# Kernel tuning notes

Hardware: AMD Instinct MI355X
Metric: run time of the kernel (lower is better)

Reference implementation:

```python
import jax, jax.numpy as jnp
import numpy as np

DIM = 96
HEADS = 6
WS = 8                      # window_size
OWS = int(WS * 0.5) + WS    # overlap_win_size = 12
PAD = (OWS - WS) // 2       # 2
Dd = Hh = Ww = 24
B = 1
L = Dd * Hh * Ww
MLP_H = DIM * 2
TBL = (WS + OWS - 1) ** 3   # 6859 relative-position-bias entries


def setup_inputs() -> dict:
    key = jax.random.key(0)
    ks = jax.random.split(key, 8)
    def n(k, shape, s=0.02):
        return jax.random.normal(k, shape, jnp.float32) * s
    return {
        "x": jax.random.normal(ks[0], (B, L, DIM), jnp.float32),
        "ln1_w": jnp.ones((DIM,), jnp.float32),
        "ln1_b": jnp.zeros((DIM,), jnp.float32),
        "qkv_w": n(ks[1], (3 * DIM, DIM)),
        "qkv_b": jnp.zeros((3 * DIM,), jnp.float32),
        "rpb": n(ks[2], (TBL, HEADS)),
        "proj_w": n(ks[3], (DIM, DIM)),
        "proj_b": jnp.zeros((DIM,), jnp.float32),
        "ln2_w": jnp.ones((DIM,), jnp.float32),
        "ln2_b": jnp.zeros((DIM,), jnp.float32),
        "fc1_w": n(ks[4], (MLP_H, DIM)),
        "fc1_b": jnp.zeros((MLP_H,), jnp.float32),
        "fc2_w": n(ks[5], (DIM, MLP_H)),
        "fc2_b": jnp.zeros((DIM,), jnp.float32),
        "rpi": jax.random.randint(ks[6], (WS ** 3, OWS ** 3), 0, TBL),
        "D": Dd, "H": Hh, "W": Ww,
    }


def _ln(x, w, b):
    m = jnp.mean(x, -1, keepdims=True)
    v = jnp.var(x, -1, keepdims=True)
    return (x - m) / jnp.sqrt(v + 1e-5) * w + b


def _ocab3d(x, ln1_w, ln1_b, qkv_w, qkv_b, rpb, proj_w, proj_b,
            ln2_w, ln2_b, fc1_w, fc1_b, fc2_w, fc2_b, rpi, D, H, W):
    Bz, Lz, C = x.shape
    hd = C // HEADS
    scale = hd ** -0.5
    shortcut = x

    xn = _ln(x, ln1_w, ln1_b).reshape(Bz, D, H, W, C)
    qkv = xn @ qkv_w.T + qkv_b                   # [B,D,H,W,3C]
    q = qkv[..., :C]
    kv = qkv[..., C:]                            # cat(k, v) on channels, [B,D,H,W,2C]

    nD, nH, nW = D // WS, H // WS, W // WS
    nw = nD * nH * nW

    # non-overlapping query windows -> [B*nw, WS^3, C]
    qw = q.reshape(Bz, nD, WS, nH, WS, nW, WS, C)
    qw = qw.transpose(0, 1, 3, 5, 2, 4, 6, 7).reshape(Bz * nw, WS ** 3, C)

    # overlapping kv windows via pad + strided gather (mirrors F.pad + unfold)
    kvp = jnp.pad(kv, ((0, 0), (PAD, PAD), (PAD, PAD), (PAD, PAD), (0, 0)))
    idx_d = (jnp.arange(nD) * WS)[:, None] + jnp.arange(OWS)[None, :]
    idx_h = (jnp.arange(nH) * WS)[:, None] + jnp.arange(OWS)[None, :]
    idx_w = (jnp.arange(nW) * WS)[:, None] + jnp.arange(OWS)[None, :]
    kw = kvp[:, idx_d]                 # [B,nD,OWS,Hp,Wp,2C]
    kw = kw[:, :, :, idx_h]            # [B,nD,OWS,nH,OWS,Wp,2C]
    kw = kw[:, :, :, :, :, idx_w]      # [B,nD,OWS,nH,OWS,nW,OWS,2C]
    kw = kw.transpose(0, 1, 3, 5, 2, 4, 6, 7).reshape(Bz * nw, OWS ** 3, 2 * C)
    kk, vv = kw[..., :C], kw[..., C:]

    qh = qw.reshape(-1, WS ** 3, HEADS, hd).transpose(0, 2, 1, 3) * scale
    kh = kk.reshape(-1, OWS ** 3, HEADS, hd).transpose(0, 2, 1, 3)
    vh = vv.reshape(-1, OWS ** 3, HEADS, hd).transpose(0, 2, 1, 3)

    attn = jnp.einsum('bhqd,bhkd->bhqk', qh, kh)               # [B*nw,H,512,1728]
    bias = rpb[rpi.reshape(-1)].reshape(WS ** 3, OWS ** 3, HEADS).transpose(2, 0, 1)
    attn = jax.nn.softmax(attn + bias[None], axis=-1)
    out = jnp.einsum('bhqk,bhkd->bhqd', attn, vh)
    out = out.transpose(0, 2, 1, 3).reshape(Bz * nw, WS ** 3, C)

    # window reverse -> [B, L, C]
    out = out.reshape(Bz, nD, nH, nW, WS, WS, WS, C)
    out = out.transpose(0, 1, 4, 2, 5, 3, 6, 7).reshape(Bz, D * H * W, C)

    x2 = out @ proj_w.T + proj_b + shortcut
    h1 = jax.nn.gelu(_ln(x2, ln2_w, ln2_b) @ fc1_w.T + fc1_b, approximate=False)
    return x2 + (h1 @ fc2_w.T + fc2_b)


def reference(x, ln1_w, ln1_b, qkv_w, qkv_b, rpb, proj_w, proj_b,
              ln2_w, ln2_b, fc1_w, fc1_b, fc2_w, fc2_b, rpi, D, H, W):
    return _ocab3d(x, ln1_w, ln1_b, qkv_w, qkv_b, rpb, proj_w, proj_b,
                   ln2_w, ln2_b, fc1_w, fc1_b, fc2_w, fc2_b, rpi, D, H, W)
```

## Files before the change

kernel.cpp:

```cpp
#include <hip/hip_runtime.h>
#include <math.h>

#define DIMC   96
#define NHEADS 6
#define HD     16
#define WSZ    8
#define OWSZ   12
#define PADW   2
#define DD     24
#define LTOK   13824
#define NWIN   27
#define NKEY   1728
#define NROW   512
#define MLPH   192
#define PDIM   28
#define PD3    21952
#define KVPN   (NHEADS*PD3*32)
#define TBL    6859
#define LSTR   82944
#define AOSTR  1327104

typedef __attribute__((ext_vector_type(4))) short bf16x4;
typedef __attribute__((ext_vector_type(8))) short bf16x8;
typedef __attribute__((ext_vector_type(4))) float f32x4;

__device__ __forceinline__ unsigned short bfround(float f) {
    unsigned u = __float_as_uint(f);
    return (unsigned short)((u + 0x7FFFu + ((u >> 16) & 1u)) >> 16);
}
__device__ __forceinline__ unsigned bfpack(float a, float b) {
    unsigned ua = __float_as_uint(a), ub = __float_as_uint(b);
    ua = (ua + 0x7FFFu + ((ua >> 16) & 1u)) >> 16;
    ub = (ub + 0x7FFFu + ((ub >> 16) & 1u)) >> 16;
    return ua | (ub << 16);
}
__device__ __forceinline__ uint4 pack8(const float* v) {
    uint4 u;
    u.x = bfpack(v[0], v[1]); u.y = bfpack(v[2], v[3]);
    u.z = bfpack(v[4], v[5]); u.w = bfpack(v[6], v[7]);
    return u;
}
__device__ __forceinline__ bf16x4 pack4(f32x4 p) {
    union { uint2 u; bf16x4 v; } r;
    r.u.x = __builtin_amdgcn_perm(__float_as_uint(p[1]), __float_as_uint(p[0]), 0x07060302u);
    r.u.y = __builtin_amdgcn_perm(__float_as_uint(p[3]), __float_as_uint(p[2]), 0x07060302u);
    return r.v;
}
__device__ __forceinline__ f32x4 mfma16(bf16x4 a, bf16x4 b, f32x4 c) {
#if __has_builtin(__builtin_amdgcn_mfma_f32_16x16x16bf16_1k)
    return __builtin_amdgcn_mfma_f32_16x16x16bf16_1k(a, b, c, 0, 0, 0);
#else
    bf16x8 a8 = {a[0], a[1], a[2], a[3], 0, 0, 0, 0};
    bf16x8 b8 = {b[0], b[1], b[2], b[3], 0, 0, 0, 0};
    return __builtin_amdgcn_mfma_f32_16x16x32_bf16(a8, b8, c, 0, 0, 0);
#endif
}

#define ZBLK 2058
__global__ __launch_bounds__(256) void init_kernel(
        float4* __restrict__ kvz, const float* __restrict__ rpb,
        float* __restrict__ rpbT) {
    int bx = blockIdx.x;
    if (bx < ZBLK) {
        int i = bx * 256 + threadIdx.x;
        if (i < KVPN * 2 / 16) kvz[i] = make_float4(0.f, 0.f, 0.f, 0.f);
    } else {
        int i = (bx - ZBLK) * 256 + threadIdx.x;
        if (i < TBL) {
            #pragma unroll
            for (int h = 0; h < NHEADS; ++h) rpbT[h * TBL + i] = rpb[i * NHEADS + h];
        }
    }
}

template<int KT, int MODE, bool LN, int NSPLIT>
__global__ __launch_bounds__(256) void gemm_kernel(
        const float* __restrict__ X, const float* __restrict__ W,
        const float* __restrict__ bias, const float* __restrict__ lnw,
        const float* __restrict__ lnb, const float* __restrict__ res,
        const float* __restrict__ X2, const float* __restrict__ lbuf,
        void* __restrict__ out, void* __restrict__ out2) {
    constexpr int K = KT * 32;
    __shared__ uint4 Af4[2 * KT * 4 * 16];
    __shared__ uint4 Bf4[6 * KT * 4 * 16];
    int tid  = threadIdx.x;
    int nc   = blockIdx.x % NSPLIT;
    int row0 = (blockIdx.x / NSPLIT) * 32;

    if (tid < 128) {
        int row = tid >> 2, part = tid & 3;
        int rt = row >> 4, mm = row & 15;
        if (MODE == 1) {
            int grow = row0 + row;
            const float4* a0 = (const float4*)(X  + (long)grow * 96 + part * 24);
            const float4* a1 = (const float4*)(X2 + (long)grow * 96 + part * 24);
            int ha = (part * 3) >> 1, hb = ha + 1;
            float inva = 1.f / (lbuf[grow*6 + ha] + lbuf[LSTR + grow*6 + ha]);
            float invb = 1.f / (lbuf[grow*6 + hb] + lbuf[LSTR + grow*6 + hb]);
            float v[24];
            #pragma unroll
            for (int i = 0; i < 6; ++i) {
                float4 u0 = a0[i], u1 = a1[i];
                #pragma unroll
                for (int j = 0; j < 4; ++j) {
                    int gc = part * 24 + i * 4 + j;
                    float lv = ((gc >> 4) == ha) ? inva : invb;
                    float s = (j==0?u0.x+u1.x : j==1?u0.y+u1.y : j==2?u0.z+u1.z : u0.w+u1.w);
                    v[i*4+j] = s * lv;
                }
            }
            #pragma unroll
            for (int gg = 0; gg < 3; ++gg) {
                int g = part * 3 + gg;
                int kt = g >> 2, qq = g & 3;
                Af4[((rt * KT + kt) * 4 + qq) * 16 + mm] = pack8(v + gg * 8);
            }
        } else if (LN) {
            float v[24];
            const float4* xp = (const float4*)(X + (long)(row0 + row) * K + part * 24);
            float s = 0.f, sq = 0.f;
            #pragma unroll
            for (int i = 0; i < 6; ++i) {
                float4 t = xp[i];
                v[i*4+0] = t.x; v[i*4+1] = t.y; v[i*4+2] = t.z; v[i*4+3] = t.w;
                s  += t.x + t.y + t.z + t.w;
                sq += t.x*t.x + t.y*t.y + t.z*t.z + t.w*t.w;
            }
            s  += __shfl_xor(s, 1);  s  += __shfl_xor(s, 2);
            sq += __shfl_xor(sq, 1); sq += __shfl_xor(sq, 2);
            float mean = s * (1.f / 96.f);
            float inv  = rsqrtf(sq * (1.f / 96.f) - mean * mean + 1e-5f);
            const float4* wp = (const float4*)(lnw + part * 24);
            const float4* bp = (const float4*)(lnb + part * 24);
            #pragma unroll
            for (int i = 0; i < 6; ++i) {
                float4 wv = wp[i], bv = bp[i];
                v[i*4+0] = (v[i*4+0] - mean) * inv * wv.x + bv.x;
                v[i*4+1] = (v[i*4+1] - mean) * inv * wv.y + bv.y;
                v[i*4+2] = (v[i*4+2] - mean) * inv * wv.z + bv.z;
                v[i*4+3] = (v[i*4+3] - mean) * inv * wv.w + bv.w;
            }
            #pragma unroll
            for (int gg = 0; gg < 3; ++gg) {
                int g = part * 3 + gg;
                int kt = g >> 2, qq = g & 3;
                Af4[((rt * KT + kt) * 4 + qq) * 16 + mm] = pack8(v + gg * 8);
            }
        } else {
            const float* xr = X + (long)(row0 + row) * K + part * (K / 4);
            #pragma unroll
            for (int gg = 0; gg < KT; ++gg) {
                const float4* xp = (const float4*)(xr + gg * 8);
                float v[8];
                float4 t0 = xp[0], t1 = xp[1];
                v[0]=t0.x; v[1]=t0.y; v[2]=t0.z; v[3]=t0.w;
                v[4]=t1.x; v[5]=t1.y; v[6]=t1.z; v[7]=t1.w;
                int g = part * KT + gg;
                int kt = g >> 2, qq = g & 3;
                Af4[((rt * KT + kt) * 4 + qq) * 16 + mm] = pack8(v);
            }
        }
    }

    for (int idx = tid; idx < 96 * 4 * KT; idx += 256) {
        int n = idx / (4 * KT);
        int g = idx % (4 * KT);
        const float4* wp = (const float4*)(W + (long)(nc * 96 + n) * K + g * 8);
        float v[8];
        float4 t0 = wp[0], t1 = wp[1];
        v[0]=t0.x; v[1]=t0.y; v[2]=t0.z; v[3]=t0.w;
        v[4]=t1.x; v[5]=t1.y; v[6]=t1.z; v[7]=t1.w;
        int ct = n >> 4, nn = n & 15, kt = g >> 2, qg = g & 3;
        Bf4[((ct * KT + kt) * 4 + qg) * 16 + nn] = pack8(v);
    }
    __syncthreads();

    int wave = tid >> 6, lane = tid & 63;
    int qq = lane >> 4, mI = lane & 15;
    int rt = wave & 1, cg = wave >> 1;

    f32x4 acc[3];
    #pragma unroll
    for (int j = 0; j < 3; ++j) acc[j] = (f32x4){0.f, 0.f, 0.f, 0.f};
    #pragma unroll
    for (int kt = 0; kt < KT; ++kt) {
        bf16x8 a = *(const bf16x8*)&Af4[((rt * KT + kt) * 4 + qq) * 16 + mI];
        #pragma unroll
        for (int j = 0; j < 3; ++j) {
            bf16x8 b = *(const bf16x8*)&Bf4[(((cg * 3 + j) * KT + kt) * 4 + qq) * 16 + mI];
            acc[j] = __builtin_amdgcn_mfma_f32_16x16x32_bf16(a, b, acc[j], 0, 0, 0);
        }
    }

    float bv[3];
    #pragma unroll
    for (int j = 0; j < 3; ++j) bv[j] = bias[nc * 96 + (cg * 3 + j) * 16 + mI];
    #pragma unroll
    for (int r = 0; r < 4; ++r) {
        int row = row0 + rt * 16 + qq * 4 + r;
        if (MODE == 0) {
            if (nc == 0) {
                unsigned short* op = (unsigned short*)out + (long)row * 96;
                #pragma unroll
                for (int j = 0; j < 3; ++j)
                    op[(cg * 3 + j) * 16 + mI] = bfround(0.25f * (acc[j][r] + bv[j]));
            } else {
                int d = row / 576, hh = (row / 24) % 24, w2 = row % 24;
                long pos = ((long)(d + 2) * 28 + (hh + 2)) * 28 + (w2 + 2);
                #pragma unroll
                for (int j = 0; j < 3; ++j) {
                    int head = cg * 3 + j;
                    ((unsigned short*)out2)[((long)head * PD3 + pos) * 32 +
                        (nc == 2 ? 16 : 0) + mI] = bfround(acc[j][r] + bv[j]);
                }
            }
        } else if (MODE == 1 || MODE == 3) {
            const float* rp = res + (long)row * 96;
            float* op = (float*)out + (long)row * 96;
            #pragma unroll
            for (int j = 0; j < 3; ++j)
                op[(cg * 3 + j) * 16 + mI] = acc[j][r] + bv[j] + rp[(cg * 3 + j) * 16 + mI];
        } else {
            float* op = (float*)out + (long)row * 192 + nc * 96;
            #pragma unroll
            for (int j = 0; j < 3; ++j) {
                float v = acc[j][r] + bv[j];
                op[(cg * 3 + j) * 16 + mI] = 0.5f * v * (1.f + erff(v * 0.70710678f));
            }
        }
    }
}

__global__ __launch_bounds__(256) void bias_kernel(
        const int* __restrict__ rpi, const float* __restrict__ rpbT,
        float* __restrict__ biasP) {
    int bx = blockIdx.x;
    int head = bx / 216;
    int r2 = bx % 216;
    int kt = r2 >> 1, qh = r2 & 1;
    const float* tab = rpbT + head * TBL;
    int k0 = kt * 16;
    int qi = qh * 256 + threadIdx.x;
    const int* rp = rpi + (long)qi * NKEY + k0;
    int idx[16];
    #pragma unroll
    for (int j = 0; j < 4; ++j) {
        int4 t = *(const int4*)(rp + j * 4);
        idx[j*4+0] = t.x; idx[j*4+1] = t.y; idx[j*4+2] = t.z; idx[j*4+3] = t.w;
    }
    #pragma unroll
    for (int quad = 0; quad < 4; ++quad) {
        float4 v;
        v.x = tab[idx[quad*4+0]];
        v.y = tab[idx[quad*4+1]];
        v.z = tab[idx[quad*4+2]];
        v.w = tab[idx[quad*4+3]];
        *(float4*)(biasP + ((((long)head*108 + kt)*4 + quad)*512 + qi)*4) = v;
    }
}

#define KSTR 20
#define VSTR 68
__global__ __launch_bounds__(256) void attn_kernel(
        const unsigned short* __restrict__ q, const unsigned short* __restrict__ kvp2,
        const float* __restrict__ biasP, float* __restrict__ ao,
        float* __restrict__ lbuf) {
    __shared__ unsigned short Ks[2][64 * KSTR];
    __shared__ unsigned short Vs[2][16 * VSTR];
    int bid = blockIdx.x;
    int w = bid / 48, rem = bid % 48;
    int head = rem >> 3;
    int quart = (rem >> 1) & 3, half = rem & 1;
    int wd8 = (w / 9) * 8, wh8 = ((w / 3) % 3) * 8, ww8 = (w % 3) * 8;
    int tid = threadIdx.x, wave = tid >> 6, lane = tid & 63;
    int quad = lane >> 4, m16 = lane & 15;
    int key = tid >> 2, part = tid & 3;
    int c0 = half ? 13 : 0;
    int cn = half ? 14 : 13;

    auto kvaddr = [&](int c) -> const uint4* {
        int jg = c * 64 + key;
        int i = jg / 144, jh = (jg / 12) % 12, jw = jg % 12;
        long sp = ((long)(wd8 + i) * PDIM + (wh8 + jh)) * PDIM + (ww8 + jw);
        return (const uint4*)(kvp2 + ((long)head * PD3 + sp) * 32 + part * 8);
    };
    auto writeLDS = [&](int b, uint4 v) {
        if (part < 2) {
            *(uint2*)(&Ks[b][key * KSTR + part * 8])     = make_uint2(v.x, v.y);
            *(uint2*)(&Ks[b][key * KSTR + part * 8 + 4]) = make_uint2(v.z, v.w);
        } else {
            int d0 = (part - 2) * 8;
            Vs[b][(d0+0)*VSTR + key] = (unsigned short)(v.x);
            Vs[b][(d0+1)*VSTR + key] = (unsigned short)(v.x >> 16);
            Vs[b][(d0+2)*VSTR + key] = (unsigned short)(v.y);
            Vs[b][(d0+3)*VSTR + key] = (unsigned short)(v.y >> 16);
            Vs[b][(d0+4)*VSTR + key] = (unsigned short)(v.z);
            Vs[b][(d0+5)*VSTR + key] = (unsigned short)(v.z >> 16);
            Vs[b][(d0+6)*VSTR + key] = (unsigned short)(v.w);
            Vs[b][(d0+7)*VSTR + key] = (unsigned short)(v.w >> 16);
        }
    };

    int grow[2]; bf16x4 qf[2];
    #pragma unroll
    for (int qt = 0; qt < 2; ++qt) {
        int ql = quart * 128 + wave * 32 + qt * 16 + m16;
        int ld = ql >> 6, lh = (ql >> 3) & 7, lw = ql & 7;
        grow[qt] = ((wd8 + ld) * 24 + (wh8 + lh)) * 24 + (ww8 + lw);
        qf[qt] = *(const bf16x4*)(q + (long)grow[qt] * 96 + head * 16 + quad * 4);
    }

    const float* bbase = biasP + (long)head * 884736 + quad * 2048
                         + ((quart * 128 + wave * 32 + m16) << 2);
    f32x4 bcur[2][4];
    #pragma unroll
    for (int qt = 0; qt < 2; ++qt)
        #pragma unroll
        for (int kt = 0; kt < 4; ++kt)
            bcur[qt][kt] = *(const f32x4*)(bbase + (long)(c0*4 + kt) * 8192 + qt * 64);

    writeLDS(0, *kvaddr(c0));

    f32x4 o[2];
    o[0] = (f32x4){0.f,0.f,0.f,0.f}; o[1] = (f32x4){0.f,0.f,0.f,0.f};
    float l[2] = {0.f, 0.f};
    uint4 stgn;

    #pragma unroll 1
    for (int cc = 0; cc < cn; ++cc) {
        int c = c0 + cc;
        if (cc + 1 < cn) stgn = *kvaddr(c + 1);
        __syncthreads();
        int b = cc & 1;

        bf16x4 kf[4];
        #pragma unroll
        for (int kt = 0; kt < 4; ++kt)
            kf[kt] = *(const bf16x4*)(&Ks[b][(kt * 16 + m16) * KSTR + quad * 4]);

        f32x4 S[2][4];
        #pragma unroll
        for (int qt = 0; qt < 2; ++qt)
            #pragma unroll
            for (int kt = 0; kt < 4; ++kt)
                S[qt][kt] = mfma16(kf[kt], qf[qt], bcur[qt][kt]);

        f32x4 bnxt[2][4];
        if (cc + 1 < cn) {
            const float* bp = bbase + (long)(c + 1) * 32768;
            #pragma unroll
            for (int qt = 0; qt < 2; ++qt)
                #pragma unroll
                for (int kt = 0; kt < 4; ++kt)
                    bnxt[qt][kt] = *(const f32x4*)(bp + kt * 8192 + qt * 64);
        }

        #pragma unroll
        for (int qt = 0; qt < 2; ++qt) {
            float ls = 0.f;
            #pragma unroll
            for (int kt = 0; kt < 4; ++kt)
                #pragma unroll
                for (int r = 0; r < 4; ++r) {
                    float p = __expf(S[qt][kt][r]);
                    S[qt][kt][r] = p; ls += p;
                }
            l[qt] += ls;
        }

        #pragma unroll
        for (int kt = 0; kt < 4; ++kt) {
            bf16x4 vf = *(const bf16x4*)(&Vs[b][m16 * VSTR + kt * 16 + quad * 4]);
            o[0] = mfma16(vf, pack4(S[0][kt]), o[0]);
            o[1] = mfma16(vf, pack4(S[1][kt]), o[1]);
        }

        if (cc + 1 < cn) writeLDS((cc + 1) & 1, stgn);
        #pragma unroll
        for (int qt = 0; qt < 2; ++qt)
            #pragma unroll
            for (int kt = 0; kt < 4; ++kt) bcur[qt][kt] = bnxt[qt][kt];
    }

    float* aout = ao + (long)half * AOSTR;
    float* lout = lbuf + (long)half * LSTR;
    #pragma unroll
    for (int qt = 0; qt < 2; ++qt) {
        float lq = l[qt];
        lq += __shfl_xor(lq, 16);
        lq += __shfl_xor(lq, 32);
        float4* op = (float4*)(aout + (long)grow[qt] * 96 + head * 16 + quad * 4);
        *op = make_float4(o[qt][0], o[qt][1], o[qt][2], o[qt][3]);
        if (quad == 0) lout[grow[qt] * 6 + head] = lq;
    }
}

extern "C" void kernel_launch(void* const* d_in, const int* in_sizes, int n_in,
                              void* d_out, int out_size, void* d_ws, size_t ws_size,
                              hipStream_t stream) {
    const float* x     = (const float*)d_in[0];
    const float* ln1w  = (const float*)d_in[1];
    const float* ln1b  = (const float*)d_in[2];
    const float* qkvw  = (const float*)d_in[3];
    const float* qkvb  = (const float*)d_in[4];
    const float* rpb   = (const float*)d_in[5];
    const float* projw = (const float*)d_in[6];
    const float* projb = (const float*)d_in[7];
    const float* ln2w  = (const float*)d_in[8];
    const float* ln2b  = (const float*)d_in[9];
    const float* fc1w  = (const float*)d_in[10];
    const float* fc1b  = (const float*)d_in[11];
    const float* fc2w  = (const float*)d_in[12];
    const float* fc2b  = (const float*)d_in[13];
    const int*   rpi   = (const int*)d_in[14];
    float* outp = (float*)d_out;

    float* ws = (float*)d_ws;
    float*          aop    = ws;
    unsigned short* q16    = (unsigned short*)(ws + 2654208);
    unsigned short* kvp16  = (unsigned short*)(ws + 3317760);
    float*          biasPf = ws + 5425152;
    float*          hbuf   = biasPf;
    float*          rpbT   = ws + 10733568;
    float*          lbuf   = ws + 10774722;
    float*          x2     = aop;

    init_kernel<<<ZBLK + 27, 256, 0, stream>>>((float4*)kvp16, rpb, rpbT);
    gemm_kernel<3, 0, true , 3><<<1296, 256, 0, stream>>>(x,  qkvw, qkvb, ln1w, ln1b, nullptr, nullptr, nullptr, q16, kvp16);
    bias_kernel<<<1296, 256, 0, stream>>>(rpi, rpbT, biasPf);
    attn_kernel<<<NWIN * NHEADS * 4 * 2, 256, 0, stream>>>(q16, kvp16, biasPf, aop, lbuf);
    gemm_kernel<3, 1, false, 1><<<432, 256, 0, stream>>>(aop, projw, projb, nullptr, nullptr, x, aop + AOSTR, lbuf, x2, nullptr);
    gemm_kernel<3, 2, true , 2><<<864, 256, 0, stream>>>(x2, fc1w, fc1b, ln2w, ln2b, nullptr, nullptr, nullptr, hbuf, nullptr);
    gemm_kernel<6, 3, false, 1><<<432, 256, 0, stream>>>(hbuf, fc2w, fc2b, nullptr, nullptr, x2, nullptr, nullptr, outp, nullptr);
}
```

Before: 190.9 us.

## Fuse proj/LN2/MLP into one kernel, store bias in bf16, remap attention blocks

Merges the three post-attention GEMM launches (proj+residual, LN2+fc1+GELU, fc2+residual) into one mlp_kernel that keeps x2 and the GELU activations in shared memory, so the x2 and hidden buffers no longer round-trip through global memory. The precomputed relative-position bias is now stored as bf16 instead of fp32, halving the bytes the attention kernel streams. The attention grid is also remapped so consecutive blocks on the same XCD share windows and heads, which may improve L2 reuse. The trade-offs are lower bias precision and a fused kernel with more syncs and more LDS use per block.

Measured after the change: 186.7 us. -2.2%, faster.

```diff
diff --git a/kernel.cpp b/kernel.cpp
--- a/kernel.cpp
+++ b/kernel.cpp
@@ -73,99 +73,56 @@
     }
 }
 
-template<int KT, int MODE, bool LN, int NSPLIT>
-__global__ __launch_bounds__(256) void gemm_kernel(
+template<int KT>
+__global__ __launch_bounds__(256) void qkv_kernel(
         const float* __restrict__ X, const float* __restrict__ W,
         const float* __restrict__ bias, const float* __restrict__ lnw,
-        const float* __restrict__ lnb, const float* __restrict__ res,
-        const float* __restrict__ X2, const float* __restrict__ lbuf,
-        void* __restrict__ out, void* __restrict__ out2) {
-    constexpr int K = KT * 32;
+        const float* __restrict__ lnb,
+        unsigned short* __restrict__ out, unsigned short* __restrict__ out2) {
     __shared__ uint4 Af4[2 * KT * 4 * 16];
     __shared__ uint4 Bf4[6 * KT * 4 * 16];
     int tid  = threadIdx.x;
-    int nc   = blockIdx.x % NSPLIT;
-    int row0 = (blockIdx.x / NSPLIT) * 32;
+    int nc   = blockIdx.x % 3;
+    int row0 = (blockIdx.x / 3) * 32;
 
     if (tid < 128) {
         int row = tid >> 2, part = tid & 3;
         int rt = row >> 4, mm = row & 15;
-        if (MODE == 1) {
-            int grow = row0 + row;
-            const float4* a0 = (const float4*)(X  + (long)grow * 96 + part * 24);
-            const float4* a1 = (const float4*)(X2 + (long)grow * 96 + part * 24);
-            int ha = (part * 3) >> 1, hb = ha + 1;
-            float inva = 1.f / (lbuf[grow*6 + ha] + lbuf[LSTR + grow*6 + ha]);
-            float invb = 1.f / (lbuf[grow*6 + hb] + lbuf[LSTR + grow*6 + hb]);
-            float v[24];
-            #pragma unroll
-            for (int i = 0; i < 6; ++i) {
-                float4 u0 = a0[i], u1 = a1[i];
-                #pragma unroll
-                for (int j = 0; j < 4; ++j) {
-                    int gc = part * 24 + i * 4 + j;
-                    float lv = ((gc >> 4) == ha) ? inva : invb;
-                    float s = (j==0?u0.x+u1.x : j==1?u0.y+u1.y : j==2?u0.z+u1.z : u0.w+u1.w);
-                    v[i*4+j] = s * lv;
-                }
-            }
-            #pragma unroll
-            for (int gg = 0; gg < 3; ++gg) {
-                int g = part * 3 + gg;
-                int kt = g >> 2, qq = g & 3;
-                Af4[((rt * KT + kt) * 4 + qq) * 16 + mm] = pack8(v + gg * 8);
-            }
-        } else if (LN) {
-            float v[24];
-            const float4* xp = (const float4*)(X + (long)(row0 + row) * K + part * 24);
-            float s = 0.f, sq = 0.f;
-            #pragma unroll
-            for (int i = 0; i < 6; ++i) {
-                float4 t = xp[i];
-                v[i*4+0] = t.x; v[i*4+1] = t.y; v[i*4+2] = t.z; v[i*4+3] = t.w;
-                s  += t.x + t.y + t.z + t.w;
-                sq += t.x*t.x + t.y*t.y + t.z*t.z + t.w*t.w;
-            }
-            s  += __shfl_xor(s, 1);  s  += __shfl_xor(s, 2);
-            sq += __shfl_xor(sq, 1); sq += __shfl_xor(sq, 2);
-            float mean = s * (1.f / 96.f);
-            float inv  = rsqrtf(sq * (1.f / 96.f) - mean * mean + 1e-5f);
-            const float4* wp = (const float4*)(lnw + part * 24);
-            const float4* bp = (const float4*)(lnb + part * 24);
-            #pragma unroll
-            for (int i = 0; i < 6; ++i) {
-                float4 wv = wp[i], bv = bp[i];
-                v[i*4+0] = (v[i*4+0] - mean) * inv * wv.x + bv.x;
-                v[i*4+1] = (v[i*4+1] - mean) * inv * wv.y + bv.y;
-                v[i*4+2] = (v[i*4+2] - mean) * inv * wv.z + bv.z;
-                v[i*4+3] = (v[i*4+3] - mean) * inv * wv.w + bv.w;
-            }
-            #pragma unroll
-            for (int gg = 0; gg < 3; ++gg) {
-                int g = part * 3 + gg;
-                int kt = g >> 2, qq = g & 3;
-                Af4[((rt * KT + kt) * 4 + qq) * 16 + mm] = pack8(v + gg * 8);
-            }
-        } else {
-            const float* xr = X + (long)(row0 + row) * K + part * (K / 4);
-            #pragma unroll
-            for (int gg = 0; gg < KT; ++gg) {
-                const float4* xp = (const float4*)(xr + gg * 8);
-                float v[8];
-                float4 t0 = xp[0], t1 = xp[1];
-                v[0]=t0.x; v[1]=t0.y; v[2]=t0.z; v[3]=t0.w;
-                v[4]=t1.x; v[5]=t1.y; v[6]=t1.z; v[7]=t1.w;
-                int g = part * KT + gg;
-                int kt = g >> 2, qq = g & 3;
-                Af4[((rt * KT + kt) * 4 + qq) * 16 + mm] = pack8(v);
-            }
-        }
-    }
-
+        float v[24];
+        const float4* xp = (const float4*)(X + (long)(row0 + row) * 96 + part * 24);
+        float s = 0.f, sq = 0.f;
+        #pragma unroll
+        for (int i = 0; i < 6; ++i) {
+            float4 t = xp[i];
+            v[i*4+0] = t.x; v[i*4+1] = t.y; v[i*4+2] = t.z; v[i*4+3] = t.w;
+            s  += t.x + t.y + t.z + t.w;
+            sq += t.x*t.x + t.y*t.y + t.z*t.z + t.w*t.w;
+        }
+        s  += __shfl_xor(s, 1);  s  += __shfl_xor(s, 2);
+        sq += __shfl_xor(sq, 1); sq += __shfl_xor(sq, 2);
+        float mean = s * (1.f / 96.f);
+        float inv  = rsqrtf(sq * (1.f / 96.f) - mean * mean + 1e-5f);
+        const float4* wp = (const float4*)(lnw + part * 24);
+        const float4* bp = (const float4*)(lnb + part * 24);
+        #pragma unroll
+        for (int i = 0; i < 6; ++i) {
+            float4 wv = wp[i], bv = bp[i];
+            v[i*4+0] = (v[i*4+0] - mean) * inv * wv.x + bv.x;
+            v[i*4+1] = (v[i*4+1] - mean) * inv * wv.y + bv.y;
+            v[i*4+2] = (v[i*4+2] - mean) * inv * wv.z + bv.z;
+            v[i*4+3] = (v[i*4+3] - mean) * inv * wv.w + bv.w;
+        }
+        #pragma unroll
+        for (int gg = 0; gg < 3; ++gg) {
+            int g = part * 3 + gg;
+            int kt = g >> 2, qq = g & 3;
+            Af4[((rt * KT + kt) * 4 + qq) * 16 + mm] = pack8(v + gg * 8);
+        }
+    }
     for (int idx = tid; idx < 96 * 4 * KT; idx += 256) {
         int n = idx / (4 * KT);
         int g = idx % (4 * KT);
-        const float4* wp = (const float4*)(W + (long)(nc * 96 + n) * K + g * 8);
+        const float4* wp = (const float4*)(W + (long)(nc * 96 + n) * 96 + g * 8);
         float v[8];
         float4 t0 = wp[0], t1 = wp[1];
         v[0]=t0.x; v[1]=t0.y; v[2]=t0.z; v[3]=t0.w;
@@ -198,34 +155,19 @@
     #pragma unroll
     for (int r = 0; r < 4; ++r) {
         int row = row0 + rt * 16 + qq * 4 + r;
-        if (MODE == 0) {
-            if (nc == 0) {
-                unsigned short* op = (unsigned short*)out + (long)row * 96;
-                #pragma unroll
-                for (int j = 0; j < 3; ++j)
-                    op[(cg * 3 + j) * 16 + mI] = bfround(0.25f * (acc[j][r] + bv[j]));
-            } else {
-                int d = row / 576, hh = (row / 24) % 24, w2 = row % 24;
-                long pos = ((long)(d + 2) * 28 + (hh + 2)) * 28 + (w2 + 2);
-                #pragma unroll
-                for (int j = 0; j < 3; ++j) {
-                    int head = cg * 3 + j;
-                    ((unsigned short*)out2)[((long)head * PD3 + pos) * 32 +
-                        (nc == 2 ? 16 : 0) + mI] = bfround(acc[j][r] + bv[j]);
-                }
-            }
-        } else if (MODE == 1 || MODE == 3) {
-            const float* rp = res + (long)row * 96;
-            float* op = (float*)out + (long)row * 96;
+        if (nc == 0) {
+            unsigned short* op = out + (long)row * 96;
             #pragma unroll
             for (int j = 0; j < 3; ++j)
-                op[(cg * 3 + j) * 16 + mI] = acc[j][r] + bv[j] + rp[(cg * 3 + j) * 16 + mI];
+                op[(cg * 3 + j) * 16 + mI] = bfround(0.25f * (acc[j][r] + bv[j]));
         } else {
-            float* op = (float*)out + (long)row * 192 + nc * 96;
+            int d = row / 576, hh = (row / 24) % 24, w2 = row % 24;
+            long pos = ((long)(d + 2) * 28 + (hh + 2)) * 28 + (w2 + 2);
             #pragma unroll
             for (int j = 0; j < 3; ++j) {
-                float v = acc[j][r] + bv[j];
-                op[(cg * 3 + j) * 16 + mI] = 0.5f * v * (1.f + erff(v * 0.70710678f));
+                int head = cg * 3 + j;
+                out2[((long)head * PD3 + pos) * 32 +
+                     (nc == 2 ? 16 : 0) + mI] = bfround(acc[j][r] + bv[j]);
             }
         }
     }
@@ -233,7 +175,7 @@
 
 __global__ __launch_bounds__(256) void bias_kernel(
         const int* __restrict__ rpi, const float* __restrict__ rpbT,
-        float* __restrict__ biasP) {
+        unsigned short* __restrict__ biasP) {
     int bx = blockIdx.x;
     int head = bx / 216;
     int r2 = bx % 216;
@@ -250,12 +192,12 @@
     }
     #pragma unroll
     for (int quad = 0; quad < 4; ++quad) {
-        float4 v;
-        v.x = tab[idx[quad*4+0]];
-        v.y = tab[idx[quad*4+1]];
-        v.z = tab[idx[quad*4+2]];
-        v.w = tab[idx[quad*4+3]];
-        *(float4*)(biasP + ((((long)head*108 + kt)*4 + quad)*512 + qi)*4) = v;
+        ushort4 v;
+        v.x = bfround(tab[idx[quad*4+0]]);
+        v.y = bfround(tab[idx[quad*4+1]]);
+        v.z = bfround(tab[idx[quad*4+2]]);
+        v.w = bfround(tab[idx[quad*4+3]]);
+        *(ushort4*)(biasP + ((((long)head*108 + kt)*4 + quad)*512 + qi)*4) = v;
     }
 }
 
@@ -263,14 +205,19 @@
 #define VSTR 68
 __global__ __launch_bounds__(256) void attn_kernel(
         const unsigned short* __restrict__ q, const unsigned short* __restrict__ kvp2,
-        const float* __restrict__ biasP, float* __restrict__ ao,
+        const unsigned short* __restrict__ biasP, float* __restrict__ ao,
         float* __restrict__ lbuf) {
     __shared__ unsigned short Ks[2][64 * KSTR];
     __shared__ unsigned short Vs[2][16 * VSTR];
     int bid = blockIdx.x;
-    int w = bid / 48, rem = bid % 48;
-    int head = rem >> 3;
-    int quart = (rem >> 1) & 3, half = rem & 1;
+    int xcd = bid & 7, slot = bid >> 3;
+    int L = xcd * 162 + slot;
+    int head = L / 216;
+    int rem = L % 216;
+    int half = rem / 108;
+    int r3 = rem % 108;
+    int quart = r3 / 27;
+    int w = r3 % 27;
     int wd8 = (w / 9) * 8, wh8 = ((w / 3) % 3) * 8, ww8 = (w % 3) * 8;
     int tid = threadIdx.x, wave = tid >> 6, lane = tid & 63;
     int quad = lane >> 4, m16 = lane & 15;
@@ -310,14 +257,14 @@
         qf[qt] = *(const bf16x4*)(q + (long)grow[qt] * 96 + head * 16 + quad * 4);
     }
 
-    const float* bbase = biasP + (long)head * 884736 + quad * 2048
-                         + ((quart * 128 + wave * 32 + m16) << 2);
-    f32x4 bcur[2][4];
+    const unsigned short* bbase = biasP + (long)head * 884736 + quad * 2048
+                                  + ((quart * 128 + wave * 32 + m16) << 2);
+    uint2 bcur[2][4];
     #pragma unroll
     for (int qt = 0; qt < 2; ++qt)
         #pragma unroll
         for (int kt = 0; kt < 4; ++kt)
-            bcur[qt][kt] = *(const f32x4*)(bbase + (long)(c0*4 + kt) * 8192 + qt * 64);
+            bcur[qt][kt] = *(const uint2*)(bbase + (long)(c0*4 + kt) * 8192 + qt * 64);
 
     writeLDS(0, *kvaddr(c0));
 
@@ -342,17 +289,24 @@
         #pragma unroll
         for (int qt = 0; qt < 2; ++qt)
             #pragma unroll
-            for (int kt = 0; kt < 4; ++kt)
-                S[qt][kt] = mfma16(kf[kt], qf[qt], bcur[qt][kt]);
-
-        f32x4 bnxt[2][4];
+            for (int kt = 0; kt < 4; ++kt) {
+                uint2 bv = bcur[qt][kt];
+                f32x4 ci;
+                ci[0] = __uint_as_float(bv.x << 16);
+                ci[1] = __uint_as_float(bv.x & 0xffff0000u);
+                ci[2] = __uint_as_float(bv.y << 16);
+                ci[3] = __uint_as_float(bv.y & 0xffff0000u);
+                S[qt][kt] = mfma16(kf[kt], qf[qt], ci);
+            }
+
+        uint2 bnxt[2][4];
         if (cc + 1 < cn) {
-            const float* bp = bbase + (long)(c + 1) * 32768;
+            const unsigned short* bp = bbase + (long)(c + 1) * 32768;
             #pragma unroll
             for (int qt = 0; qt < 2; ++qt)
                 #pragma unroll
                 for (int kt = 0; kt < 4; ++kt)
-                    bnxt[qt][kt] = *(const f32x4*)(bp + kt * 8192 + qt * 64);
+                    bnxt[qt][kt] = *(const uint2*)(bp + kt * 8192 + qt * 64);
         }
 
         #pragma unroll
@@ -392,6 +346,216 @@
         float4* op = (float4*)(aout + (long)grow[qt] * 96 + head * 16 + quad * 4);
         *op = make_float4(o[qt][0], o[qt][1], o[qt][2], o[qt][3]);
         if (quad == 0) lout[grow[qt] * 6 + head] = lq;
+    }
+}
+
+__global__ __launch_bounds__(256) void mlp_kernel(
+        const float* __restrict__ ao0, const float* __restrict__ ao1,
+        const float* __restrict__ lbuf,
+        const float* __restrict__ projw, const float* __restrict__ projb,
+        const float* __restrict__ x,
+        const float* __restrict__ ln2w, const float* __restrict__ ln2b,
+        const float* __restrict__ fc1w, const float* __restrict__ fc1b,
+        const float* __restrict__ fc2w, const float* __restrict__ fc2b,
+        float* __restrict__ out) {
+    __shared__ uint4 Af4[2 * 3 * 4 * 16];
+    __shared__ uint4 Bf4[6 * 3 * 4 * 16];
+    __shared__ float x2s[32 * 96];
+    __shared__ unsigned short h16[32 * 192];
+    int tid = threadIdx.x;
+    int row0 = blockIdx.x * 32;
+    int wave = tid >> 6, lane = tid & 63;
+    int qq = lane >> 4, mI = lane & 15;
+    int rt = wave & 1, cg = wave >> 1;
+
+    if (tid < 128) {
+        int row = tid >> 2, part = tid & 3;
+        int rtA = row >> 4, mm = row & 15;
+        int grow = row0 + row;
+        const float4* a0 = (const float4*)(ao0 + (long)grow * 96 + part * 24);
+        const float4* a1 = (const float4*)(ao1 + (long)grow * 96 + part * 24);
+        int ha = (part * 3) >> 1, hb = ha + 1;
+        float inva = 1.f / (lbuf[grow*6 + ha] + lbuf[LSTR + grow*6 + ha]);
+        float invb = 1.f / (lbuf[grow*6 + hb] + lbuf[LSTR + grow*6 + hb]);
+        float v[24];
+        #pragma unroll
+        for (int i = 0; i < 6; ++i) {
+            float4 u0 = a0[i], u1 = a1[i];
+            #pragma unroll
+            for (int j = 0; j < 4; ++j) {
+                int gc = part * 24 + i * 4 + j;
+                float lv = ((gc >> 4) == ha) ? inva : invb;
+                float s = (j==0?u0.x+u1.x : j==1?u0.y+u1.y : j==2?u0.z+u1.z : u0.w+u1.w);
+                v[i*4+j] = s * lv;
+            }
+        }
+        #pragma unroll
+        for (int gg = 0; gg < 3; ++gg) {
+            int g = part * 3 + gg;
+            int kt = g >> 2, q4 = g & 3;
+            Af4[((rtA * 3 + kt) * 4 + q4) * 16 + mm] = pack8(v + gg * 8);
+        }
+    }
+    for (int idx = tid; idx < 96 * 12; idx += 256) {
+        int n = idx / 12, g = idx % 12;
+        const float4* wp = (const float4*)(projw + (long)n * 96 + g * 8);
+        float v[8];
+        float4 t0 = wp[0], t1 = wp[1];
+        v[0]=t0.x; v[1]=t0.y; v[2]=t0.z; v[3]=t0.w;
+        v[4]=t1.x; v[5]=t1.y; v[6]=t1.z; v[7]=t1.w;
+        int ct = n >> 4, nn = n & 15, kt = g >> 2, qg = g & 3;
+        Bf4[((ct * 3 + kt) * 4 + qg) * 16 + nn] = pack8(v);
+    }
+    __syncthreads();
+
+    {
+        f32x4 acc[3];
+        #pragma unroll
+        for (int j = 0; j < 3; ++j) acc[j] = (f32x4){0.f,0.f,0.f,0.f};
+        #pragma unroll
+        for (int kt = 0; kt < 3; ++kt) {
+            bf16x8 a = *(const bf16x8*)&Af4[((rt * 3 + kt) * 4 + qq) * 16 + mI];
+            #pragma unroll
+            for (int j = 0; j < 3; ++j) {
+                bf16x8 b = *(const bf16x8*)&Bf4[(((cg * 3 + j) * 3 + kt) * 4 + qq) * 16 + mI];
+                acc[j] = __builtin_amdgcn_mfma_f32_16x16x32_bf16(a, b, acc[j], 0, 0, 0);
+            }
+        }
+        float bv[3];
+        #pragma unroll
+        for (int j = 0; j < 3; ++j) bv[j] = projb[(cg * 3 + j) * 16 + mI];
+        #pragma unroll
+        for (int r = 0; r < 4; ++r) {
+            int row = rt * 16 + qq * 4 + r;
+            int grow = row0 + row;
+            #pragma unroll
+            for (int j = 0; j < 3; ++j) {
+                int col = (cg * 3 + j) * 16 + mI;
+                x2s[row * 96 + col] = acc[j][r] + bv[j] + x[(long)grow * 96 + col];
+            }
+        }
+    }
+    __syncthreads();
+
+    if (tid < 128) {
+        int row = tid >> 2, part = tid & 3;
+        int rtA = row >> 4, mm = row & 15;
+        float v[24];
+        const float4* xp = (const float4*)(x2s + row * 96 + part * 24);
+        float s = 0.f, sq = 0.f;
+        #pragma unroll
+        for (int i = 0; i < 6; ++i) {
+            float4 t = xp[i];
+            v[i*4+0] = t.x; v[i*4+1] = t.y; v[i*4+2] = t.z; v[i*4+3] = t.w;
+            s  += t.x + t.y + t.z + t.w;
+            sq += t.x*t.x + t.y*t.y + t.z*t.z + t.w*t.w;
+        }
+        s  += __shfl_xor(s, 1);  s  += __shfl_xor(s, 2);
+        sq += __shfl_xor(sq, 1); sq += __shfl_xor(sq, 2);
+        float mean = s * (1.f / 96.f);
+        float inv  = rsqrtf(sq * (1.f / 96.f) - mean * mean + 1e-5f);
+        const float4* wp = (const float4*)(ln2w + part * 24);
+        const float4* bp = (const float4*)(ln2b + part * 24);
+        #pragma unroll
+        for (int i = 0; i < 6; ++i) {
+            float4 wv = wp[i], bv = bp[i];
+            v[i*4+0] = (v[i*4+0] - mean) * inv * wv.x + bv.x;
+            v[i*4+1] = (v[i*4+1] - mean) * inv * wv.y + bv.y;
+            v[i*4+2] = (v[i*4+2] - mean) * inv * wv.z + bv.z;
+            v[i*4+3] = (v[i*4+3] - mean) * inv * wv.w + bv.w;
+        }
+        #pragma unroll
+        for (int gg = 0; gg < 3; ++gg) {
+            int g = part * 3 + gg;
+            int kt = g >> 2, q4 = g & 3;
+            Af4[((rtA * 3 + kt) * 4 + q4) * 16 + mm] = pack8(v + gg * 8);
+        }
+    }
+
+    #pragma unroll 1
+    for (int nc = 0; nc < 2; ++nc) {
+        if (nc) __syncthreads();
+        for (int idx = tid; idx < 96 * 12; idx += 256) {
+            int n = idx / 12, g = idx % 12;
+            const float4* wp = (const float4*)(fc1w + (long)(nc * 96 + n) * 96 + g * 8);
+            float v[8];
+            float4 t0 = wp[0], t1 = wp[1];
+            v[0]=t0.x; v[1]=t0.y; v[2]=t0.z; v[3]=t0.w;
+            v[4]=t1.x; v[5]=t1.y; v[6]=t1.z; v[7]=t1.w;
+            int ct = n >> 4, nn = n & 15, kt = g >> 2, qg = g & 3;
+            Bf4[((ct * 3 + kt) * 4 + qg) * 16 + nn] = pack8(v);
+        }
+        __syncthreads();
+
+        f32x4 acc[3];
+        #pragma unroll
+        for (int j = 0; j < 3; ++j) acc[j] = (f32x4){0.f,0.f,0.f,0.f};
+        #pragma unroll
+        for (int kt = 0; kt < 3; ++kt) {
+            bf16x8 a = *(const bf16x8*)&Af4[((rt * 3 + kt) * 4 + qq) * 16 + mI];
+            #pragma unroll
+            for (int j = 0; j < 3; ++j) {
+                bf16x8 b = *(const bf16x8*)&Bf4[(((cg * 3 + j) * 3 + kt) * 4 + qq) * 16 + mI];
+                acc[j] = __builtin_amdgcn_mfma_f32_16x16x32_bf16(a, b, acc[j], 0, 0, 0);
+            }
+        }
+        float bv[3];
+        #pragma unroll
+        for (int j = 0; j < 3; ++j) bv[j] = fc1b[nc * 96 + (cg * 3 + j) * 16 + mI];
+        #pragma unroll
+        for (int r = 0; r < 4; ++r) {
+            int row = rt * 16 + qq * 4 + r;
+            #pragma unroll
+            for (int j = 0; j < 3; ++j) {
+                int col = nc * 96 + (cg * 3 + j) * 16 + mI;
+                float v = acc[j][r] + bv[j];
+                float g = 0.5f * v * (1.f + erff(v * 0.70710678f));
+                int fi = (((row >> 4) * 6 + (col >> 5)) * 4 + ((col >> 3) & 3)) * 16 + (row & 15);
+                h16[fi * 8 + (col & 7)] = bfround(g);
+            }
+        }
+    }
+
+    f32x4 acc2[3];
+    #pragma unroll
+    for (int j = 0; j < 3; ++j) acc2[j] = (f32x4){0.f,0.f,0.f,0.f};
+    #pragma unroll 1
+    for (int kh = 0; kh < 2; ++kh) {
+        __syncthreads();
+        for (int idx = tid; idx < 96 * 12; idx += 256) {
+            int n = idx / 12, g = idx % 12;
+            const float4* wp = (const float4*)(fc2w + (long)n * 192 + kh * 96 + g * 8);
+            float v[8];
+            float4 t0 = wp[0], t1 = wp[1];
+            v[0]=t0.x; v[1]=t0.y; v[2]=t0.z; v[3]=t0.w;
+            v[4]=t1.x; v[5]=t1.y; v[6]=t1.z; v[7]=t1.w;
+            int ct = n >> 4, nn = n & 15, kt = g >> 2, qg = g & 3;
+            Bf4[((ct * 3 + kt) * 4 + qg) * 16 + nn] = pack8(v);
+        }
+        __syncthreads();
+        #pragma unroll
+        for (int kt = 0; kt < 3; ++kt) {
+            int ktA = kh * 3 + kt;
+            bf16x8 a = *(const bf16x8*)&h16[(((rt * 6 + ktA) * 4 + qq) * 16 + mI) * 8];
+            #pragma unroll
+            for (int j = 0; j < 3; ++j) {
+                bf16x8 b = *(const bf16x8*)&Bf4[(((cg * 3 + j) * 3 + kt) * 4 + qq) * 16 + mI];
+                acc2[j] = __builtin_amdgcn_mfma_f32_16x16x32_bf16(a, b, acc2[j], 0, 0, 0);
+            }
+        }
+    }
+    float bv[3];
+    #pragma unroll
+    for (int j = 0; j < 3; ++j) bv[j] = fc2b[(cg * 3 + j) * 16 + mI];
+    #pragma unroll
+    for (int r = 0; r < 4; ++r) {
+        int row = rt * 16 + qq * 4 + r;
+        int grow = row0 + row;
+        #pragma unroll
+        for (int j = 0; j < 3; ++j) {
+            int col = (cg * 3 + j) * 16 + mI;
+            out[(long)grow * 96 + col] = acc2[j][r] + bv[j] + x2s[row * 96 + col];
+        }
     }
 }
 
@@ -419,17 +583,14 @@
     float*          aop    = ws;
     unsigned short* q16    = (unsigned short*)(ws + 2654208);
     unsigned short* kvp16  = (unsigned short*)(ws + 3317760);
-    float*          biasPf = ws + 5425152;
-    float*          hbuf   = biasPf;
-    float*          rpbT   = ws + 10733568;
-    float*          lbuf   = ws + 10774722;
-    float*          x2     = aop;
+    unsigned short* biasP  = (unsigned short*)(ws + 5425152);
+    float*          rpbT   = ws + 8079360;
+    float*          lbuf   = ws + 8120514;
 
     init_kernel<<<ZBLK + 27, 256, 0, stream>>>((float4*)kvp16, rpb, rpbT);
-    gemm_kernel<3, 0, true , 3><<<1296, 256, 0, stream>>>(x,  qkvw, qkvb, ln1w, ln1b, nullptr, nullptr, nullptr, q16, kvp16);
-    bias_kernel<<<1296, 256, 0, stream>>>(rpi, rpbT, biasPf);
-    attn_kernel<<<NWIN * NHEADS * 4 * 2, 256, 0, stream>>>(q16, kvp16, biasPf, aop, lbuf);
-    gemm_kernel<3, 1, false, 1><<<432, 256, 0, stream>>>(aop, projw, projb, nullptr, nullptr, x, aop + AOSTR, lbuf, x2, nullptr);
-    gemm_kernel<3, 2, true , 2><<<864, 256, 0, stream>>>(x2, fc1w, fc1b, ln2w, ln2b, nullptr, nullptr, nullptr, hbuf, nullptr);
-    gemm_kernel<6, 3, false, 1><<<432, 256, 0, stream>>>(hbuf, fc2w, fc2b, nullptr, nullptr, x2, nullptr, nullptr, outp, nullptr);
-}
+    qkv_kernel<3><<<1296, 256, 0, stream>>>(x, qkvw, qkvb, ln1w, ln1b, q16, kvp16);
+    bias_kernel<<<1296, 256, 0, stream>>>(rpi, rpbT, biasP);
+    attn_kernel<<<NWIN * NHEADS * 4 * 2, 256, 0, stream>>>(q16, kvp16, biasP, aop, lbuf);
+    mlp_kernel<<<432, 256, 0, stream>>>(aop, aop + AOSTR, lbuf, projw, projb, x,
+                                        ln2w, ln2b, fc1w, fc1b, fc2w, fc2b, outp);
+}
```
